# Kernel tuning notes

Measured on AMD Instinct MI355X. Metric: run time of the kernel, lower is better.

The kernel has to match this reference:

```python
import jax, jax.numpy as jnp
import numpy as np

D = 128  # input_depth == output_depth
NUM_NODES_PATTERN = np.tile(np.array([32, 48, 64, 96], dtype=np.int64), 64)  # G=256 graphs


def _build_indices(nn_np):
    """Per pair-entry (row-major within each n_g x n_g block): global row node,
    global col node, graph id, diagonal mask; plus per-node graph id / size."""
    G = len(nn_np)
    offs = np.zeros(G, dtype=np.int64)
    offs[1:] = np.cumsum(nn_np)[:-1]
    rows_l, cols_l, g_l, diag_l = [], [], [], []
    for gi, (n, o) in enumerate(zip(nn_np, offs)):
        i = np.repeat(np.arange(n, dtype=np.int64), n)  # row index within block
        j = np.tile(np.arange(n, dtype=np.int64), n)    # col index within block
        rows_l.append(o + i)
        cols_l.append(o + j)
        g_l.append(np.full(n * n, gi, dtype=np.int64))
        diag_l.append(i == j)
    rows = np.concatenate(rows_l)
    cols = np.concatenate(cols_l)
    g_edge = np.concatenate(g_l)
    diag = np.concatenate(diag_l)
    g_node = np.repeat(np.arange(G, dtype=np.int64), nn_np)  # graph of each node
    n_node = np.repeat(nn_np, nn_np)                          # n_g of each node
    N = int(nn_np.sum())
    return rows, cols, g_edge, diag, g_node, n_node, N, G


def setup_inputs() -> dict:
    key = jax.random.key(0)
    nn_np = NUM_NODES_PATTERN
    E = int(np.sum(nn_np ** 2))  # 1,064,960 pair entries
    N = int(nn_np.sum())         # 15,360 nodes
    k1, k2, k3 = jax.random.split(key, 3)
    x = jax.random.normal(k1, (E, D), dtype=jnp.float32)
    coeffs = jax.random.normal(k2, (D, D, 5), dtype=jnp.float32) * float(np.sqrt(2.0) / (D + D))
    bias = jnp.zeros((1, D), dtype=jnp.float32)
    edges_index = jax.random.randint(k3, (2, E), 0, N, dtype=jnp.int64)  # unused by the layer
    num_nodes = jnp.asarray(nn_np)
    return {"x": x, "coeffs": coeffs, "bias": bias,
            "edges_index": edges_index, "num_nodes": num_nodes}


def reference(x, coeffs, bias, edges_index, num_nodes):
    # edges_index is unused, matching the original forward.
    nn_np = np.asarray(num_nodes)
    rows, cols, g_edge, diag, g_node, n_node, N, G = _build_indices(nn_np)
    seg = jax.ops.segment_sum
    diag_m = jnp.asarray(diag)[:, None].astype(x.dtype)  # [E,1]
    n = jnp.asarray(n_node).astype(x.dtype)[:, None]     # [N,1] block size per node

    op1 = seg(x * diag_m, jnp.asarray(rows), num_segments=N)          # diag part (unnormalized)
    op3 = seg(x, jnp.asarray(rows), num_segments=N) / n               # row sums / n
    op4 = seg(x, jnp.asarray(cols), num_segments=N) / n               # col sums / n
    diag_g = seg(x * diag_m, jnp.asarray(g_edge), num_segments=G)     # [G,d] trace per graph
    all_g = seg(x, jnp.asarray(g_edge), num_segments=G)               # [G,d] total sum per graph
    gn = jnp.asarray(g_node)
    op2 = diag_g[gn] / n                                              # trace broadcast / n
    op5 = all_g[gn] / (n * n)                                         # total broadcast / n^2

    ops = jnp.stack([op1, op2, op3, op4, op5], axis=2)                # [N, d, 5]
    out = jnp.einsum('dsb,ndb->ns', coeffs, ops) + bias               # [N, output_depth]
    return out
```

## Files before the change

### kernel.cpp

```cpp
#include <hip/hip_runtime.h>

#define D 128


template<int CTRL>
__device__ __forceinline__ float f_dpp_add(float v) {
    return v + __int_as_float(__builtin_amdgcn_update_dpp(
        0, __float_as_int(v), CTRL, 0xF, 0xF, true));
}

#define DPP_ROR8 0x128

__device__ __forceinline__ float f_xor16_sum(float v) {
#if __has_builtin(__builtin_amdgcn_permlane16_swap)
    typedef int v2i __attribute__((ext_vector_type(2)));
    v2i r = __builtin_amdgcn_permlane16_swap(__float_as_int(v), __float_as_int(v),
                                             false, false);
    return __int_as_float(r[0]) + __int_as_float(r[1]);
#else
    return v + __shfl_xor(v, 16);
#endif
}

__device__ __forceinline__ float f_xor32_sum(float v) {
#if __has_builtin(__builtin_amdgcn_permlane32_swap)
    typedef int v2i __attribute__((ext_vector_type(2)));
    v2i r = __builtin_amdgcn_permlane32_swap(__float_as_int(v), __float_as_int(v),
                                             false, false);
    return __int_as_float(r[0]) + __int_as_float(r[1]);
#else
    return v + __shfl_xor(v, 32);
#endif
}

__device__ __forceinline__ void f4add(float4& a, const float4& b) {
    a.x += b.x; a.y += b.y; a.z += b.z; a.w += b.w;
}

__device__ __forceinline__ void f4_jreduce_full(float4& a) {
    a.x = f_dpp_add<DPP_ROR8>(a.x);
    a.y = f_dpp_add<DPP_ROR8>(a.y);
    a.z = f_dpp_add<DPP_ROR8>(a.z);
    a.w = f_dpp_add<DPP_ROR8>(a.w);
    a.x = f_xor16_sum(a.x);
    a.y = f_xor16_sum(a.y);
    a.z = f_xor16_sum(a.z);
    a.w = f_xor16_sum(a.w);
    a.x = f_xor32_sum(a.x);
    a.y = f_xor32_sum(a.y);
    a.z = f_xor32_sum(a.z);
    a.w = f_xor32_sum(a.w);
}

template<int N>
__device__ __forceinline__ void run_class(const float* __restrict__ x,
                                          long ebase, int o, int gidx, int chunk,
                                          float* __restrict__ diagG,
                                          float* __restrict__ rowG,
                                          float* __restrict__ colG,
                                          float* __restrict__ trG,
                                          float* __restrict__ totG,
                                          float4* __restrict__ rowtile ,
                                          float4* __restrict__ red     ) {
    constexpr int NW = (N < 64 ? N / 8 : 8);
    const int tid = threadIdx.x;
    const int l   = tid & 63;
    const int w   = tid >> 6;
    const int f4  = l & 7;
    const int j0  = tid >> 3;
    constexpr bool TWO = (N > 64);
    const bool act0 = (j0 < N);
    const bool act1 = TWO && (w < 4);
    const float invn = 1.0f / (float)N;

    const float4* x4 = reinterpret_cast<const float4*>(x);
    const long istride = (long)N * 32;
    const long e0 = (ebase + j0) * 32 + chunk * 8 + f4;

    float4 c0 = {0,0,0,0}, c1 = {0,0,0,0};

    int buf = 0;
    for (int t0 = 0; t0 < N; t0 += 16, buf ^= 1) {
        if (act0) {
            const float4* p0 = x4 + e0 + (long)t0 * istride;
            const float4* p1 = p0 + 64L * 32;
            float4* wt = rowtile + ((buf * 16) * 8 + w) * 8 + f4;
#pragma unroll 2
            for (int r = 0; r < 16; ++r) {
                float4 v = p0[(long)r * istride];
                f4add(c0, v);
                if (TWO && act1) {
                    float4 u = p1[(long)r * istride];
                    f4add(c1, u);
                    f4add(v, u);
                }
                f4_jreduce_full(v);
                if (l < 8) wt[r * 64] = v;
            }
        }
        __syncthreads();
        {
            const int rr = tid >> 5;
            const int dd = tid & 31;
            const float* rp = reinterpret_cast<const float*>(rowtile)
                            + (buf * 16 + rr) * 256 + dd;
            float acc = 0.f;
#pragma unroll
            for (int w2 = 0; w2 < NW; ++w2) acc += rp[w2 * 32];
            rowG[(long)(o + t0 + rr) * D + chunk * 32 + dd] = acc * invn;
        }
    }

    float4 d0 = {0,0,0,0}, d1 = {0,0,0,0};
    if (act0) d0 = x4[e0 + (long)j0 * istride];
    if (TWO && act1) d1 = x4[e0 + 64L * 32 + (long)(j0 + 64) * istride];

    float4* diag4 = reinterpret_cast<float4*>(diagG);
    float4* col4  = reinterpret_cast<float4*>(colG);
    if (act0) {
        diag4[(long)(o + j0) * 32 + chunk * 8 + f4] = d0;
        col4 [(long)(o + j0) * 32 + chunk * 8 + f4] = c0;
    }
    if (TWO && act1) {
        diag4[(long)(o + j0 + 64) * 32 + chunk * 8 + f4] = d1;
        col4 [(long)(o + j0 + 64) * 32 + chunk * 8 + f4] = c1;
    }

    {
        float4 td = d0; if (TWO) f4add(td, d1);
        float4 tc = c0; if (TWO) f4add(tc, c1);
        f4_jreduce_full(td);
        f4_jreduce_full(tc);
        if (l < 8) {
            red[w * 8 + f4]      = td;
            red[64 + w * 8 + f4] = tc;
        }
    }
    __syncthreads();
    float4* tr4  = reinterpret_cast<float4*>(trG);
    float4* tot4 = reinterpret_cast<float4*>(totG);
    if (tid < 8) {
        float4 a = {0,0,0,0};
#pragma unroll
        for (int w2 = 0; w2 < NW; ++w2) f4add(a, red[w2 * 8 + tid]);
        tr4[gidx * 32 + chunk * 8 + tid] = a;
    } else if (tid < 16) {
        const int f = tid - 8;
        float4 a = {0,0,0,0};
#pragma unroll
        for (int w2 = 0; w2 < NW; ++w2) f4add(a, red[64 + w2 * 8 + f]);
        tot4[gidx * 32 + chunk * 8 + f] = a;
    }
}

__global__ __launch_bounds__(512, 8) void k1_reduce(const float* __restrict__ x,
                                                    float* __restrict__ diagG,
                                                    float* __restrict__ rowG,
                                                    float* __restrict__ colG,
                                                    float* __restrict__ trG,
                                                    float* __restrict__ totG) {
    __shared__ float4 rowtile[2048];
    __shared__ float4 red[128];

    const int b  = blockIdx.x;
    const int bb = b & 255;
    const int k  = bb >> 2;
    const int chunk = bb & 3;

    if (b < 256) {
        run_class<96>(x, 16640L * k + 7424, 240 * k + 144, 4 * k + 3, chunk, diagG, rowG, colG, trG, totG, rowtile, red);
    } else if (b < 512) {
        run_class<64>(x, 16640L * k + 3328, 240 * k + 80, 4 * k + 2, chunk, diagG, rowG, colG, trG, totG, rowtile, red);
    } else if (b < 768) {
        run_class<48>(x, 16640L * k + 1024, 240 * k + 32, 4 * k + 1, chunk, diagG, rowG, colG, trG, totG, rowtile, red);
    } else {
        run_class<32>(x, 16640L * k, 240 * k, 4 * k, chunk, diagG, rowG, colG, trG, totG, rowtile, red);
    }
}

__global__ void k0_transpose(const float* __restrict__ coeffs, float* __restrict__ Wt) {
    int d = blockIdx.x;
    int s = threadIdx.x;
    const float* cp = coeffs + ((long)d * D + s) * 5;
#pragma unroll
    for (int b = 0; b < 5; ++b) Wt[b * (D * D) + d * D + s] = cp[b];
}

__global__ __launch_bounds__(128) void k2_pg(const float* __restrict__ trG,
                                             const float* __restrict__ totG,
                                             const float* __restrict__ Wt,
                                             const float* __restrict__ bias,
                                             float* __restrict__ pg) {
    __shared__ float tr[D], tt[D];
    const int ns_[4] = {32, 48, 64, 96};
    int g = blockIdx.x;
    int c = g & 3;
    float invn = 1.0f / (float)ns_[c];

    int s = threadIdx.x;
    tr[s] = trG[g * D + s] * invn;
    tt[s] = totG[g * D + s] * invn * invn;
    __syncthreads();

    const float* W1 = Wt + 1 * D * D;
    const float* W4 = Wt + 4 * D * D;
    float acc = 0.f;
#pragma unroll 4
    for (int dd = 0; dd < D; ++dd)
        acc += W1[dd * D + s] * tr[dd] + W4[dd * D + s] * tt[dd];
    pg[g * D + s] = bias[s] + acc;
}

__global__ __launch_bounds__(512) void k3_gemm(const float* __restrict__ diagG,
                                               const float* __restrict__ rowG,
                                               const float* __restrict__ colG,
                                               const float* __restrict__ Wt,
                                               const float* __restrict__ pg,
                                               float* __restrict__ out) {
    __shared__ __align__(16) float ash[3][64][D];
    __shared__ int gish[64];
    const int nd0 = blockIdx.x * 64;
    const int tid = threadIdx.x;

    const float4* diag4 = reinterpret_cast<const float4*>(diagG);
    const float4* row4  = reinterpret_cast<const float4*>(rowG);
    const float4* col4  = reinterpret_cast<const float4*>(colG);

    for (int idx = tid; idx < 64 * 32; idx += 512) {
        int nn = idx >> 5;
        int q  = idx & 31;
        int nd = nd0 + nn;
        int p  = nd / 240;
        int r  = nd - p * 240;
        int c, n;
        if (r < 32)       { c = 0; n = 32; }
        else if (r < 80)  { c = 1; n = 48; }
        else if (r < 144) { c = 2; n = 64; }
        else              { c = 3; n = 96; }
        float invn = 1.0f / (float)n;
        float4 dv = diag4[(long)nd * 32 + q];
        float4 rv = row4[(long)nd * 32 + q];
        float4 cv = col4[(long)nd * 32 + q];
        cv.x *= invn; cv.y *= invn; cv.z *= invn; cv.w *= invn;
        *reinterpret_cast<float4*>(&ash[0][nn][q * 4]) = dv;
        *reinterpret_cast<float4*>(&ash[1][nn][q * 4]) = rv;
        *reinterpret_cast<float4*>(&ash[2][nn][q * 4]) = cv;
        if (q == 0) gish[nn] = 4 * p + c;
    }
    __syncthreads();

    const int s4 = tid & 31;
    const int nq = tid >> 5;
    const float* W0 = Wt;
    const float* W2 = Wt + 2 * D * D;
    const float* W3 = Wt + 3 * D * D;

    float4 acc[4];
#pragma unroll
    for (int a = 0; a < 4; ++a) acc[a] = make_float4(0.f, 0.f, 0.f, 0.f);

    for (int d4 = 0; d4 < 32; ++d4) {
        float4 w0[4], w2[4], w3[4];
#pragma unroll
        for (int dd = 0; dd < 4; ++dd) {
            const int d = d4 * 4 + dd;
            w0[dd] = *reinterpret_cast<const float4*>(&W0[d * D + s4 * 4]);
            w2[dd] = *reinterpret_cast<const float4*>(&W2[d * D + s4 * 4]);
            w3[dd] = *reinterpret_cast<const float4*>(&W3[d * D + s4 * 4]);
        }
#pragma unroll
        for (int a = 0; a < 4; ++a) {
            const int nn = nq * 4 + a;
            float4 a0 = *reinterpret_cast<const float4*>(&ash[0][nn][d4 * 4]);
            float4 a1 = *reinterpret_cast<const float4*>(&ash[1][nn][d4 * 4]);
            float4 a2 = *reinterpret_cast<const float4*>(&ash[2][nn][d4 * 4]);
            const float* a0f = reinterpret_cast<const float*>(&a0);
            const float* a1f = reinterpret_cast<const float*>(&a1);
            const float* a2f = reinterpret_cast<const float*>(&a2);
#pragma unroll
            for (int dd = 0; dd < 4; ++dd) {
                acc[a].x += w0[dd].x * a0f[dd] + w2[dd].x * a1f[dd] + w3[dd].x * a2f[dd];
                acc[a].y += w0[dd].y * a0f[dd] + w2[dd].y * a1f[dd] + w3[dd].y * a2f[dd];
                acc[a].z += w0[dd].z * a0f[dd] + w2[dd].z * a1f[dd] + w3[dd].z * a2f[dd];
                acc[a].w += w0[dd].w * a0f[dd] + w2[dd].w * a1f[dd] + w3[dd].w * a2f[dd];
            }
        }
    }

#pragma unroll
    for (int a = 0; a < 4; ++a) {
        const int nn = nq * 4 + a;
        const int nd = nd0 + nn;
        const int g  = gish[nn];
        float4 pgv = *reinterpret_cast<const float4*>(&pg[g * D + s4 * 4]);
        float4 r_;
        r_.x = acc[a].x + pgv.x;
        r_.y = acc[a].y + pgv.y;
        r_.z = acc[a].z + pgv.z;
        r_.w = acc[a].w + pgv.w;
        *reinterpret_cast<float4*>(&out[(long)nd * D + s4 * 4]) = r_;
    }
}

extern "C" void kernel_launch(void* const* d_in, const int* in_sizes, int n_in,
                              void* d_out, int out_size, void* d_ws, size_t ws_size,
                              hipStream_t stream) {
    const float* x      = (const float*)d_in[0];
    const float* coeffs = (const float*)d_in[1];
    const float* bias   = (const float*)d_in[2];

    float* ws    = (float*)d_ws;
    float* Wt    = ws;
    float* diagG = Wt + 81920;
    float* rowG  = diagG + 1966080;
    float* colG  = rowG + 1966080;
    float* pg    = colG + 1966080;
    float* trG   = pg + 32768;
    float* totG  = trG + 32768;
    float* out   = (float*)d_out;

    k0_transpose<<<128, 128, 0, stream>>>(coeffs, Wt);
    k1_reduce<<<1024, 512, 0, stream>>>(x, diagG, rowG, colG, trG, totG);
    k2_pg<<<256, 128, 0, stream>>>(trG, totG, Wt, bias, pg);
    k3_gemm<<<240, 512, 0, stream>>>(diagG, rowG, colG, Wt, pg, out);
}
```

Measured before the change: 203.3 us.

## Spread N=96 second-half columns across all waves and remap block-to-graph order

```diff
diff --git a/kernel.cpp b/kernel.cpp
--- a/kernel.cpp
+++ b/kernel.cpp
@@ -50,6 +50,17 @@
     a.y = f_xor32_sum(a.y);
     a.z = f_xor32_sum(a.z);
     a.w = f_xor32_sum(a.w);
+}
+
+__device__ __forceinline__ void f4_jreduce4(float4& a) {
+    a.x = f_dpp_add<DPP_ROR8>(a.x);
+    a.y = f_dpp_add<DPP_ROR8>(a.y);
+    a.z = f_dpp_add<DPP_ROR8>(a.z);
+    a.w = f_dpp_add<DPP_ROR8>(a.w);
+    a.x = f_xor16_sum(a.x);
+    a.y = f_xor16_sum(a.y);
+    a.z = f_xor16_sum(a.z);
+    a.w = f_xor16_sum(a.w);
 }
 
 template<int N>
@@ -70,12 +81,14 @@
     const int j0  = tid >> 3;
     constexpr bool TWO = (N > 64);
     const bool act0 = (j0 < N);
-    const bool act1 = TWO && (w < 4);
+    const bool actB = TWO && (l < 32);
+    const int  jB   = TWO ? (64 + w * 4 + ((l >> 3) & 3)) : 0;
     const float invn = 1.0f / (float)N;
 
     const float4* x4 = reinterpret_cast<const float4*>(x);
     const long istride = (long)N * 32;
     const long e0 = (ebase + j0) * 32 + chunk * 8 + f4;
+    const long eB = (ebase + jB) * 32 + chunk * 8 + f4;
 
     float4 c0 = {0,0,0,0}, c1 = {0,0,0,0};
 
@@ -83,19 +96,22 @@
     for (int t0 = 0; t0 < N; t0 += 16, buf ^= 1) {
         if (act0) {
             const float4* p0 = x4 + e0 + (long)t0 * istride;
-            const float4* p1 = p0 + 64L * 32;
+            const float4* pB = x4 + eB + (long)t0 * istride;
             float4* wt = rowtile + ((buf * 16) * 8 + w) * 8 + f4;
 #pragma unroll 2
             for (int r = 0; r < 16; ++r) {
                 float4 v = p0[(long)r * istride];
                 f4add(c0, v);
-                if (TWO && act1) {
-                    float4 u = p1[(long)r * istride];
+                float4 s = v;
+                f4_jreduce_full(s);
+                if (TWO) {
+                    float4 u = {0,0,0,0};
+                    if (actB) u = pB[(long)r * istride];
                     f4add(c1, u);
-                    f4add(v, u);
+                    f4_jreduce4(u);
+                    f4add(s, u);
                 }
-                f4_jreduce_full(v);
-                if (l < 8) wt[r * 64] = v;
+                if (l < 8) wt[r * 64] = s;
             }
         }
         __syncthreads();
@@ -111,9 +127,9 @@
         }
     }
 
-    float4 d0 = {0,0,0,0}, d1 = {0,0,0,0};
+    float4 d0 = {0,0,0,0}, dB = {0,0,0,0};
     if (act0) d0 = x4[e0 + (long)j0 * istride];
-    if (TWO && act1) d1 = x4[e0 + 64L * 32 + (long)(j0 + 64) * istride];
+    if (actB) dB = x4[eB + (long)jB * istride];
 
     float4* diag4 = reinterpret_cast<float4*>(diagG);
     float4* col4  = reinterpret_cast<float4*>(colG);
@@ -121,14 +137,14 @@
         diag4[(long)(o + j0) * 32 + chunk * 8 + f4] = d0;
         col4 [(long)(o + j0) * 32 + chunk * 8 + f4] = c0;
     }
-    if (TWO && act1) {
-        diag4[(long)(o + j0 + 64) * 32 + chunk * 8 + f4] = d1;
-        col4 [(long)(o + j0 + 64) * 32 + chunk * 8 + f4] = c1;
+    if (actB) {
+        diag4[(long)(o + jB) * 32 + chunk * 8 + f4] = dB;
+        col4 [(long)(o + jB) * 32 + chunk * 8 + f4] = c1;
     }
 
     {
-        float4 td = d0; if (TWO) f4add(td, d1);
-        float4 tc = c0; if (TWO) f4add(tc, c1);
+        float4 td = d0, tc = c0;
+        if (TWO) { f4add(td, dB); f4add(tc, c1); }
         f4_jreduce_full(td);
         f4_jreduce_full(tc);
         if (l < 8) {
@@ -153,19 +169,19 @@
     }
 }
 
-__global__ __launch_bounds__(512, 8) void k1_reduce(const float* __restrict__ x,
-                                                    float* __restrict__ diagG,
-                                                    float* __restrict__ rowG,
-                                                    float* __restrict__ colG,
-                                                    float* __restrict__ trG,
-                                                    float* __restrict__ totG) {
+__global__ __launch_bounds__(512) void k1_reduce(const float* __restrict__ x,
+                                                 float* __restrict__ diagG,
+                                                 float* __restrict__ rowG,
+                                                 float* __restrict__ colG,
+                                                 float* __restrict__ trG,
+                                                 float* __restrict__ totG) {
     __shared__ float4 rowtile[2048];
     __shared__ float4 red[128];
 
-    const int b  = blockIdx.x;
-    const int bb = b & 255;
-    const int k  = bb >> 2;
-    const int chunk = bb & 3;
+    const int b     = blockIdx.x;
+    const int local = b & 255;
+    const int k     = (local & 7) | ((local >> 5) << 3);
+    const int chunk = (local >> 3) & 3;
 
     if (b < 256) {
         run_class<96>(x, 16640L * k + 7424, 240 * k + 144, 4 * k + 3, chunk, diagG, rowG, colG, trG, totG, rowtile, red);
```

New measurement: 207.8 us. +2.2%, slower.
